# Kernel optimization log

Hardware: AMD Instinct MI355X
Metric: run time of the kernel (lower is better)

## Reference

```python
import jax, jax.numpy as jnp
import numpy as np

N_NODES = 50000
IN_DIM = 128
HID = 64
HEADS = 4
N_EDGES = 800000


def setup_inputs() -> dict:
    key = jax.random.key(0)
    ks = jax.random.split(key, 16)
    x = jax.random.normal(ks[0], (N_NODES, IN_DIM), dtype=jnp.float32)
    edge_index = jax.random.randint(ks[1], (2, N_EDGES), 0, N_NODES, dtype=jnp.int32)
    s = 0.1
    # layer 0: IN_DIM -> HEADS*HID (concat)
    W0 = jax.random.normal(ks[2], (IN_DIM, HEADS * HID), dtype=jnp.float32) * s
    a_src0 = jax.random.normal(ks[3], (HEADS, HID), dtype=jnp.float32) * s
    a_dst0 = jax.random.normal(ks[4], (HEADS, HID), dtype=jnp.float32) * s
    b0 = jnp.zeros((HEADS * HID,), dtype=jnp.float32)
    # layer 1: HEADS*HID -> HEADS*HID (concat)
    W1 = jax.random.normal(ks[5], (HEADS * HID, HEADS * HID), dtype=jnp.float32) * s
    a_src1 = jax.random.normal(ks[6], (HEADS, HID), dtype=jnp.float32) * s
    a_dst1 = jax.random.normal(ks[7], (HEADS, HID), dtype=jnp.float32) * s
    b1 = jnp.zeros((HEADS * HID,), dtype=jnp.float32)
    # layer 2: HEADS*HID -> HID (heads=1, concat=False)
    W2 = jax.random.normal(ks[8], (HEADS * HID, HID), dtype=jnp.float32) * s
    a_src2 = jax.random.normal(ks[9], (1, HID), dtype=jnp.float32) * s
    a_dst2 = jax.random.normal(ks[10], (1, HID), dtype=jnp.float32) * s
    b2 = jnp.zeros((HID,), dtype=jnp.float32)
    return {"x": x, "edge_index": edge_index,
            "W0": W0, "a_src0": a_src0, "a_dst0": a_dst0, "b0": b0,
            "W1": W1, "a_src1": a_src1, "a_dst1": a_dst1, "b1": b1,
            "W2": W2, "a_src2": a_src2, "a_dst2": a_dst2, "b2": b2}


def gat_conv(h_in, src, dst, W, a_src, a_dst, b, concat):
    """PyG-style GATConv (eval mode, self-loops already appended to src/dst)."""
    H, C = a_src.shape
    n = h_in.shape[0]
    h = (h_in @ W).reshape(n, H, C)                       # [N,H,C]
    alpha_s = jnp.sum(h * a_src[None], axis=-1)            # [N,H]
    alpha_d = jnp.sum(h * a_dst[None], axis=-1)            # [N,H]
    e = jax.nn.leaky_relu(alpha_s[src] + alpha_d[dst], 0.2)  # [E,H]
    # segment softmax over destination neighborhoods (numerically stable)
    m = jax.ops.segment_max(e, dst, num_segments=n)        # [N,H]
    m = jnp.where(jnp.isfinite(m), m, 0.0)
    ex = jnp.exp(e - m[dst])
    denom = jax.ops.segment_sum(ex, dst, num_segments=n)
    alpha = ex / (denom[dst] + 1e-16)                      # [E,H]
    msg = h[src] * alpha[:, :, None]                       # [E,H,C]
    out = jax.ops.segment_sum(msg, dst, num_segments=n)    # [N,H,C]
    out = out.reshape(n, H * C) if concat else out.mean(axis=1)
    return out + b


def reference(x, edge_index, W0, a_src0, a_dst0, b0, W1, a_src1, a_dst1, b1, W2, a_src2, a_dst2, b2):
    n = x.shape[0]
    loops = jnp.arange(n, dtype=edge_index.dtype)
    src = jnp.concatenate([edge_index[0], loops])  # add self-loops (PyG default)
    dst = jnp.concatenate([edge_index[1], loops])
    h = gat_conv(x, src, dst, W0, a_src0, a_dst0, b0, concat=True)
    h = jax.nn.elu(h)
    h = gat_conv(h, src, dst, W1, a_src1, a_dst1, b1, concat=True)
    h = jax.nn.elu(h)
    h = gat_conv(h, src, dst, W2, a_src2, a_dst2, b2, concat=False)
    return h  # [N, HID]
```

## Files before the change

### kernel.cpp

```cpp
#include <hip/hip_runtime.h>
#include <hip/hip_bf16.h>

typedef __hip_bfloat16 bf16;
typedef short s8v __attribute__((ext_vector_type(8)));
typedef float f32x4 __attribute__((ext_vector_type(4)));

__device__ __forceinline__ unsigned short f2bf_bits(float x) {
    union { bf16 h; unsigned short u; } v; v.h = __float2bfloat16(x); return v.u;
}
__device__ __forceinline__ float bfbits2f(unsigned short u) {
    union { unsigned u32; float f; } v; v.u32 = ((unsigned)u) << 16; return v.f;
}

template<typename T>
__device__ __forceinline__ void gload_lds16(const T* g, T* l) {
    __builtin_amdgcn_global_load_lds(
        (const __attribute__((address_space(1))) unsigned int*)g,
        (__attribute__((address_space(3))) unsigned int*)l, 16, 0, 0);
}

__device__ __forceinline__ uint4 load8(const bf16* p) { return *(const uint4*)p; }

__global__ void convert_kernel(const float* __restrict__ x, bf16* __restrict__ xb, int total4) {
    int i = blockIdx.x * blockDim.x + threadIdx.x;
    if (i >= total4) return;
    float4 f = *(const float4*)(x + (size_t)i * 4);
    union { uint2 u; unsigned short us[4]; } cv;
    cv.us[0] = f2bf_bits(f.x); cv.us[1] = f2bf_bits(f.y);
    cv.us[2] = f2bf_bits(f.z); cv.us[3] = f2bf_bits(f.w);
    *(uint2*)(xb + (size_t)i * 4) = cv.u;
}

__device__ __forceinline__ void tr1(const float* W, bf16* Wt, int idx, int K, int N) {
    int nn = idx / K, k = idx - nn * K;
    Wt[idx] = __float2bfloat16(W[(size_t)k * N + nn]);
}
__global__ void transpose_all_kernel(const float* __restrict__ W0, const float* __restrict__ W1,
                                     const float* __restrict__ W2, bf16* __restrict__ wt0,
                                     bf16* __restrict__ wt1, bf16* __restrict__ wt2) {
    int idx = blockIdx.x * blockDim.x + threadIdx.x;
    if (idx < 32768) tr1(W0, wt0, idx, 128, 256);
    else if (idx < 32768 + 65536) tr1(W1, wt1, idx - 32768, 256, 256);
    else if (idx < 32768 + 65536 + 16384) tr1(W2, wt2, idx - 98304, 256, 64);
}

__global__ void hist_kernel(const int* __restrict__ dst, int* counts, int E, int n) {
    int i = blockIdx.x * blockDim.x + threadIdx.x;
    if (i < E) {
        int d = dst[i];
        if ((unsigned)d < (unsigned)n) atomicAdd(&counts[d], 1);
    }
}

__global__ __launch_bounds__(1024) void scan_phase1(
        const int* __restrict__ counts, int* __restrict__ excl_out,
        int* __restrict__ blocksums, int n) {
    __shared__ int wsum[16];
    __shared__ int woff[16];
    int tid = threadIdx.x, lane = tid & 63, wid = tid >> 6;
    int i = blockIdx.x * 1024 + tid;
    int v = (i < n) ? counts[i] + 1 : 0;
    int incl = v;
    #pragma unroll
    for (int d = 1; d < 64; d <<= 1) {
        int t = __shfl_up(incl, d, 64);
        if (lane >= d) incl += t;
    }
    if (lane == 63) wsum[wid] = incl;
    __syncthreads();
    if (wid == 0) {
        int wv = (lane < 16) ? wsum[lane] : 0;
        int wincl = wv;
        #pragma unroll
        for (int d = 1; d < 16; d <<= 1) {
            int t = __shfl_up(wincl, d, 64);
            if (lane >= d) wincl += t;
        }
        if (lane < 16) woff[lane] = wincl - wv;
    }
    __syncthreads();
    if (i < n) excl_out[i] = woff[wid] + incl - v;
    if (tid == 1023) blocksums[blockIdx.x] = woff[15] + wsum[15];
}

__global__ __launch_bounds__(1024) void scan_phase2(
        const int* __restrict__ blocksums, int* __restrict__ row_ptr,
        int* __restrict__ cursor, int nb, int n) {
    int tid = threadIdx.x, lane = tid & 63;
    int i = blockIdx.x * 1024 + tid;
    int v = (lane < nb) ? blocksums[lane] : 0;
    int incl = v;
    #pragma unroll
    for (int d = 1; d < 64; d <<= 1) {
        int t = __shfl_up(incl, d, 64);
        if (lane >= d) incl += t;
    }
    int excl_lane = incl - v;
    int base = __shfl(excl_lane, blockIdx.x, 64);
    int total = __shfl(incl, nb - 1, 64);
    if (i < n) {
        int val = row_ptr[i] + base;
        row_ptr[i] = val;
        cursor[i] = val;
    }
    if (blockIdx.x == 0 && tid == 0) row_ptr[n] = total;
}

__global__ void scatter_kernel(const int* __restrict__ src, const int* __restrict__ dst,
                               int* cursor, int* col_src, int E, int n) {
    int i = blockIdx.x * blockDim.x + threadIdx.x;
    if (i < E) {
        int d = dst[i];
        if ((unsigned)d >= (unsigned)n) return;
        int s = src[i];
        if ((unsigned)s >= (unsigned)n) s = d;
        int pos = atomicAdd(&cursor[d], 1);
        col_src[pos] = s;
    } else if (i < E + n) {
        int v = i - E;
        int pos = atomicAdd(&cursor[v], 1);
        col_src[pos] = v;
    }
}

__global__ __launch_bounds__(256) void gemm128_kernel(
        const bf16* __restrict__ A, const bf16* __restrict__ Wt, bf16* __restrict__ C,
        const float* __restrict__ a_src, const float* __restrict__ a_dst,
        float* __restrict__ asb, float* __restrict__ adb,
        int M, int K, int N, int H) {
    __shared__ __align__(16) bf16 As[128 * 64];
    __shared__ __align__(16) bf16 Bs[128 * 64];
    int tid = threadIdx.x;
    int w = tid >> 6, l = tid & 63;
    int lm = l & 15, quad = l >> 4;
    int m0 = blockIdx.x * 128, n0 = blockIdx.y * 128;
    int wr = (w >> 1) * 64, wc = (w & 1) * 64;
    int srow = w * 32 + (l >> 3);
    int schunk = l & 7;
    f32x4 acc[4][4] = {};
    for (int kt = 0; kt < K; kt += 64) {
        #pragma unroll
        for (int j = 0; j < 4; ++j) {
            int row = srow + j * 8;
            int g = schunk ^ (row & 7);
            int m = m0 + row; if (m >= M) m = M - 1;
            gload_lds16(A + (size_t)m * K + kt + g * 8, As + row * 64 + schunk * 8);
            gload_lds16(Wt + (size_t)(n0 + row) * K + kt + g * 8, Bs + row * 64 + schunk * 8);
        }
        __syncthreads();
        #pragma unroll
        for (int ks = 0; ks < 2; ++ks) {
            s8v a[4], b[4];
            #pragma unroll
            for (int mi = 0; mi < 4; ++mi) {
                int row = wr + mi * 16 + lm;
                int c = (ks * 4 + quad) ^ (row & 7);
                a[mi] = *(const s8v*)(As + row * 64 + c * 8);
            }
            #pragma unroll
            for (int ni = 0; ni < 4; ++ni) {
                int row = wc + ni * 16 + lm;
                int c = (ks * 4 + quad) ^ (row & 7);
                b[ni] = *(const s8v*)(Bs + row * 64 + c * 8);
            }
            #pragma unroll
            for (int mi = 0; mi < 4; ++mi)
                #pragma unroll
                for (int ni = 0; ni < 4; ++ni)
                    acc[mi][ni] = __builtin_amdgcn_mfma_f32_16x16x32_bf16(
                        a[mi], b[ni], acc[mi][ni], 0, 0, 0);
        }
        __syncthreads();
    }
    int head = (n0 + wc) >> 6;
    float a_s[4], a_d[4];
    #pragma unroll
    for (int ni = 0; ni < 4; ++ni) {
        int col = n0 + wc + ni * 16 + lm;
        a_s[ni] = a_src[col];
        a_d[ni] = a_dst[col];
    }
    #pragma unroll
    for (int mi = 0; mi < 4; ++mi) {
        #pragma unroll
        for (int reg = 0; reg < 4; ++reg) {
            int m = m0 + wr + mi * 16 + quad * 4 + reg;
            float ps = 0.f, pd = 0.f;
            #pragma unroll
            for (int ni = 0; ni < 4; ++ni) {
                float v = acc[mi][ni][reg];
                ps += v * a_s[ni];
                pd += v * a_d[ni];
                if (m < M)
                    C[(size_t)m * N + n0 + wc + ni * 16 + lm] = __float2bfloat16(v);
            }
            #pragma unroll
            for (int d = 1; d < 16; d <<= 1) {
                ps += __shfl_xor(ps, d, 64);
                pd += __shfl_xor(pd, d, 64);
            }
            if (lm == 0 && m < M) {
                atomicAdd(&asb[(size_t)m * H + head], ps);
                atomicAdd(&adb[(size_t)m * H + head], pd);
            }
        }
    }
}

__global__ __launch_bounds__(256) void gemm64_kernel(
        const bf16* __restrict__ A, const bf16* __restrict__ Wt, bf16* __restrict__ C,
        const float* __restrict__ a_src, const float* __restrict__ a_dst,
        float* __restrict__ asb, float* __restrict__ adb,
        int M, int K, int N) {
    __shared__ __align__(16) bf16 As[64][72];
    __shared__ __align__(16) bf16 Bs[64][72];
    int tid = threadIdx.x;
    int m0 = blockIdx.x * 64;
    int w = tid >> 6;
    int l = tid & 63;
    int lm = l & 15;
    int quad = l >> 4;
    int r = tid >> 2;
    int kb = (tid & 3) * 8;
    f32x4 acc[4] = {};
    int mstage = m0 + r;
    for (int kt = 0; kt < K; kt += 64) {
        #pragma unroll
        for (int c = 0; c < 2; ++c) {
            int kk = kb + c * 32;
            uint4 av = (mstage < M) ? load8(&A[(size_t)mstage * K + kt + kk])
                                    : make_uint4(0, 0, 0, 0);
            *(uint4*)&As[r][kk] = av;
            *(uint4*)&Bs[r][kk] = load8(&Wt[(size_t)r * K + kt + kk]);
        }
        __syncthreads();
        #pragma unroll
        for (int ks = 0; ks < 2; ++ks) {
            s8v a = *(const s8v*)&As[w * 16 + lm][ks * 32 + quad * 8];
            #pragma unroll
            for (int nb = 0; nb < 4; ++nb) {
                s8v b = *(const s8v*)&Bs[nb * 16 + lm][ks * 32 + quad * 8];
                acc[nb] = __builtin_amdgcn_mfma_f32_16x16x32_bf16(a, b, acc[nb], 0, 0, 0);
            }
        }
        __syncthreads();
    }
    float a_s[4], a_d[4];
    #pragma unroll
    for (int nb = 0; nb < 4; ++nb) {
        a_s[nb] = a_src[nb * 16 + lm];
        a_d[nb] = a_dst[nb * 16 + lm];
    }
    #pragma unroll
    for (int reg = 0; reg < 4; ++reg) {
        int m = m0 + w * 16 + quad * 4 + reg;
        float ps = 0.f, pd = 0.f;
        #pragma unroll
        for (int nb = 0; nb < 4; ++nb) {
            float v = acc[nb][reg];
            ps += v * a_s[nb];
            pd += v * a_d[nb];
            if (m < M)
                C[(size_t)m * N + nb * 16 + lm] = __float2bfloat16(v);
        }
        #pragma unroll
        for (int d = 1; d < 16; d <<= 1) {
            ps += __shfl_xor(ps, d, 64);
            pd += __shfl_xor(pd, d, 64);
        }
        if (lm == 0 && m < M) {
            atomicAdd(&asb[m], ps);
            atomicAdd(&adb[m], pd);
        }
    }
}

template<int CTOT, int H, int VEC, typename TOUT>
__global__ __launch_bounds__(256) void agg_kernel(
        const bf16* __restrict__ hbuf,
        const float* __restrict__ as, const float* __restrict__ ad,
        const int* __restrict__ row_ptr, const int* __restrict__ col_src,
        const float* __restrict__ bias,
        TOUT* __restrict__ outp, int n, int apply_elu) {
    int lane = threadIdx.x & 63;
    int node = blockIdx.x * 4 + (threadIdx.x >> 6);
    if (node >= n) return;
    const int c0 = lane * VEC;
    const int head = c0 >> 6;
    int start = row_ptr[node], end = row_ptr[node + 1];
    float adn = ad[(size_t)node * H + head];
    float acc[VEC] = {};
    float denom = 0.f;

    auto edge_w = [&](int s) -> float {
        float x = as[(size_t)s * H + head] + adn;
        x = (x > 0.f) ? x : 0.2f * x;
        return __expf(fminf(x, 30.f));
    };
    auto loadH = [&](int s, float* o) {
        const bf16* p = hbuf + (size_t)s * CTOT + c0;
        if constexpr (VEC == 4) {
            union { uint2 u; unsigned short us[4]; } cv;
            cv.u = *(const uint2*)p;
            #pragma unroll
            for (int v = 0; v < 4; ++v) o[v] = bfbits2f(cv.us[v]);
        } else {
            o[0] = bfbits2f(*(const unsigned short*)p);
        }
    };

    int e = start;
    for (; e + 8 <= end; e += 8) {
        int s[8];
        float w[8], hv[8][VEC];
        #pragma unroll
        for (int j = 0; j < 8; ++j) {
            s[j] = col_src[e + j];
            if ((unsigned)s[j] >= (unsigned)n) s[j] = node;
        }
        #pragma unroll
        for (int j = 0; j < 8; ++j) loadH(s[j], hv[j]);
        #pragma unroll
        for (int j = 0; j < 8; ++j) w[j] = edge_w(s[j]);
        #pragma unroll
        for (int j = 0; j < 8; ++j) {
            denom += w[j];
            #pragma unroll
            for (int v = 0; v < VEC; ++v) acc[v] += w[j] * hv[j][v];
        }
    }
    for (; e < end; ++e) {
        int s = col_src[e];
        if ((unsigned)s >= (unsigned)n) s = node;
        float hv[VEC];
        loadH(s, hv);
        float w = edge_w(s);
        denom += w;
        #pragma unroll
        for (int v = 0; v < VEC; ++v) acc[v] += w * hv[v];
    }
    float inv = 1.f / (denom + 1e-16f);
    float o[VEC];
    #pragma unroll
    for (int v = 0; v < VEC; ++v) {
        o[v] = acc[v] * inv + bias[c0 + v];
        if (apply_elu) o[v] = (o[v] > 0.f) ? o[v] : (__expf(o[v]) - 1.f);
    }
    if constexpr (VEC == 4) {
        union { uint2 u; unsigned short us[4]; } cv;
        #pragma unroll
        for (int v = 0; v < 4; ++v) cv.us[v] = f2bf_bits(o[v]);
        *(uint2*)((bf16*)outp + (size_t)node * CTOT + c0) = cv.u;
    } else {
        outp[(size_t)node * CTOT + c0] = (TOUT)o[0];
    }
}

extern "C" void kernel_launch(void* const* d_in, const int* in_sizes, int n_in,
                              void* d_out, int out_size, void* d_ws, size_t ws_size,
                              hipStream_t stream) {
    const float* x   = (const float*)d_in[0];
    const int*   ei  = (const int*)d_in[1];
    const float* W0  = (const float*)d_in[2];
    const float* as0 = (const float*)d_in[3];
    const float* ad0 = (const float*)d_in[4];
    const float* b0  = (const float*)d_in[5];
    const float* W1  = (const float*)d_in[6];
    const float* as1 = (const float*)d_in[7];
    const float* ad1 = (const float*)d_in[8];
    const float* b1  = (const float*)d_in[9];
    const float* W2  = (const float*)d_in[10];
    const float* as2 = (const float*)d_in[11];
    const float* ad2 = (const float*)d_in[12];
    const float* b2  = (const float*)d_in[13];
    float* out = (float*)d_out;

    const int n = in_sizes[0] / 128;
    const int E = in_sizes[1] / 2;
    const int* esrc = ei;
    const int* edst = ei + E;

    char* ws = (char*)d_ws;
    bf16* hb0 = (bf16*)ws;
    bf16* hb1 = hb0 + (size_t)n * 256;
    bf16* xb  = hb1 + (size_t)n * 256;
    bf16* wt0 = xb + (size_t)n * 128;
    bf16* wt1 = wt0 + 128 * 256;
    bf16* wt2 = wt1 + 256 * 256;
    float* asb = (float*)(wt2 + 256 * 64);
    float* adb = asb + (size_t)n * 4;
    int* row_ptr = (int*)(adb + (size_t)n * 4);
    int* cursor  = row_ptr + (n + 64);
    int* col_src = cursor + n;
    int* blocksums = col_src + (E + n + 64);

    const int nb = (n + 1023) / 1024;

    convert_kernel<<<(n * 128 / 4 + 255) / 256, 256, 0, stream>>>(x, xb, n * 128 / 4);
    transpose_all_kernel<<<(114688 + 255) / 256, 256, 0, stream>>>(W0, W1, W2, wt0, wt1, wt2);
    hipMemsetAsync(cursor, 0, (size_t)n * sizeof(int), stream);
    hist_kernel<<<(E + 255) / 256, 256, 0, stream>>>(edst, cursor, E, n);
    scan_phase1<<<nb, 1024, 0, stream>>>(cursor, row_ptr, blocksums, n);
    scan_phase2<<<nb, 1024, 0, stream>>>(blocksums, row_ptr, cursor, nb, n);
    scatter_kernel<<<(E + n + 255) / 256, 256, 0, stream>>>(esrc, edst, cursor, col_src, E, n);

    dim3 blk(256);
    int mg128 = (n + 127) / 128;
    int mg64  = (n + 63) / 64;
    int ag = (n + 3) / 4;
    size_t alpha_bytes = (size_t)n * 8 * sizeof(float);

    hipMemsetAsync(asb, 0, alpha_bytes, stream);
    gemm128_kernel<<<dim3(mg128, 2), blk, 0, stream>>>(xb, wt0, hb0, as0, ad0,
                                                       asb, adb, n, 128, 256, 4);
    agg_kernel<256, 4, 4, bf16><<<ag, blk, 0, stream>>>(hb0, asb, adb, row_ptr, col_src,
                                                        b0, hb1, n, 1);
    hipMemsetAsync(asb, 0, alpha_bytes, stream);
    gemm128_kernel<<<dim3(mg128, 2), blk, 0, stream>>>(hb1, wt1, hb0, as1, ad1,
                                                       asb, adb, n, 256, 256, 4);
    agg_kernel<256, 4, 4, bf16><<<ag, blk, 0, stream>>>(hb0, asb, adb, row_ptr, col_src,
                                                        b1, hb1, n, 1);
    hipMemsetAsync(asb, 0, alpha_bytes, stream);
    gemm64_kernel<<<dim3(mg64, 1), blk, 0, stream>>>(hb1, wt2, hb0, as2, ad2,
                                                     asb, adb, n, 256, 64);
    agg_kernel<64, 1, 1, float><<<ag, blk, 0, stream>>>(hb0, asb, adb, row_ptr, col_src,
                                                        b2, out, n, 0);
}
```

Before: 476.9 us.

## Precompute per-edge attention weights in a separate pass before aggregation

Adds a wprep kernel that computes the leaky-ReLU/exp edge weight once per edge and head and stores it in a buffer aliased over the bf16 input copy. Previously every lane of the aggregation kernel gathered the source alpha and recomputed the exponential itself. The aggregation now reads these precomputed weights, and its unroll factor drops from 8 to 4 when each lane holds 4 channels. The cost is an extra launch per layer plus writing and re-reading about (E+N)*H floats, while the source-alpha gathers it replaces were small and likely cache-resident.

```diff
diff --git a/kernel.cpp b/kernel.cpp
--- a/kernel.cpp
+++ b/kernel.cpp
@@ -275,10 +275,33 @@
     }
 }
 
+template<int H>
+__global__ __launch_bounds__(256) void wprep_kernel(
+        const float* __restrict__ asb, const float* __restrict__ adb,
+        const int* __restrict__ row_ptr, const int* __restrict__ col_src,
+        float* __restrict__ wge, int n) {
+    int lane = threadIdx.x & 63;
+    int node = blockIdx.x * 4 + (threadIdx.x >> 6);
+    if (node >= n) return;
+    int start = row_ptr[node], end = row_ptr[node + 1];
+    float adn[H];
+    #pragma unroll
+    for (int h = 0; h < H; ++h) adn[h] = adb[(size_t)node * H + h];
+    for (int e = start + lane; e < end; e += 64) {
+        int s = col_src[e];
+        if ((unsigned)s >= (unsigned)n) s = node;
+        #pragma unroll
+        for (int h = 0; h < H; ++h) {
+            float x = asb[(size_t)s * H + h] + adn[h];
+            x = (x > 0.f) ? x : 0.2f * x;
+            wge[(size_t)e * H + h] = __expf(fminf(x, 30.f));
+        }
+    }
+}
+
 template<int CTOT, int H, int VEC, typename TOUT>
 __global__ __launch_bounds__(256) void agg_kernel(
-        const bf16* __restrict__ hbuf,
-        const float* __restrict__ as, const float* __restrict__ ad,
+        const bf16* __restrict__ hbuf, const float* __restrict__ wge,
         const int* __restrict__ row_ptr, const int* __restrict__ col_src,
         const float* __restrict__ bias,
         TOUT* __restrict__ outp, int n, int apply_elu) {
@@ -288,15 +311,9 @@
     const int c0 = lane * VEC;
     const int head = c0 >> 6;
     int start = row_ptr[node], end = row_ptr[node + 1];
-    float adn = ad[(size_t)node * H + head];
     float acc[VEC] = {};
     float denom = 0.f;
 
-    auto edge_w = [&](int s) -> float {
-        float x = as[(size_t)s * H + head] + adn;
-        x = (x > 0.f) ? x : 0.2f * x;
-        return __expf(fminf(x, 30.f));
-    };
     auto loadH = [&](int s, float* o) {
         const bf16* p = hbuf + (size_t)s * CTOT + c0;
         if constexpr (VEC == 4) {
@@ -309,21 +326,22 @@
         }
     };
 
+    constexpr int U = (VEC == 1) ? 8 : 4;
     int e = start;
-    for (; e + 8 <= end; e += 8) {
-        int s[8];
-        float w[8], hv[8][VEC];
-        #pragma unroll
-        for (int j = 0; j < 8; ++j) {
+    for (; e + U <= end; e += U) {
+        int s[U];
+        float w[U], hv[U][VEC];
+        #pragma unroll
+        for (int j = 0; j < U; ++j) {
             s[j] = col_src[e + j];
             if ((unsigned)s[j] >= (unsigned)n) s[j] = node;
         }
         #pragma unroll
-        for (int j = 0; j < 8; ++j) loadH(s[j], hv[j]);
-        #pragma unroll
-        for (int j = 0; j < 8; ++j) w[j] = edge_w(s[j]);
-        #pragma unroll
-        for (int j = 0; j < 8; ++j) {
+        for (int j = 0; j < U; ++j) w[j] = wge[(size_t)(e + j) * H + head];
+        #pragma unroll
+        for (int j = 0; j < U; ++j) loadH(s[j], hv[j]);
+        #pragma unroll
+        for (int j = 0; j < U; ++j) {
             denom += w[j];
             #pragma unroll
             for (int v = 0; v < VEC; ++v) acc[v] += w[j] * hv[j][v];
@@ -334,7 +352,7 @@
         if ((unsigned)s >= (unsigned)n) s = node;
         float hv[VEC];
         loadH(s, hv);
-        float w = edge_w(s);
+        float w = wge[(size_t)e * H + head];
         denom += w;
         #pragma unroll
         for (int v = 0; v < VEC; ++v) acc[v] += w * hv[v];
@@ -384,7 +402,9 @@
     bf16* hb0 = (bf16*)ws;
     bf16* hb1 = hb0 + (size_t)n * 256;
     bf16* xb  = hb1 + (size_t)n * 256;
-    bf16* wt0 = xb + (size_t)n * 128;
+    float* wge = (float*)xb;
+    char* after_xw = (char*)xb + ((size_t)(E + n + 64) * 4 * sizeof(float));
+    bf16* wt0 = (bf16*)after_xw;
     bf16* wt1 = wt0 + 128 * 256;
     bf16* wt2 = wt1 + 256 * 256;
     float* asb = (float*)(wt2 + 256 * 64);
@@ -413,16 +433,19 @@
     hipMemsetAsync(asb, 0, alpha_bytes, stream);
     gemm128_kernel<<<dim3(mg128, 2), blk, 0, stream>>>(xb, wt0, hb0, as0, ad0,
                                                        asb, adb, n, 128, 256, 4);
-    agg_kernel<256, 4, 4, bf16><<<ag, blk, 0, stream>>>(hb0, asb, adb, row_ptr, col_src,
+    wprep_kernel<4><<<ag, blk, 0, stream>>>(asb, adb, row_ptr, col_src, wge, n);
+    agg_kernel<256, 4, 4, bf16><<<ag, blk, 0, stream>>>(hb0, wge, row_ptr, col_src,
                                                         b0, hb1, n, 1);
     hipMemsetAsync(asb, 0, alpha_bytes, stream);
     gemm128_kernel<<<dim3(mg128, 2), blk, 0, stream>>>(hb1, wt1, hb0, as1, ad1,
                                                        asb, adb, n, 256, 256, 4);
-    agg_kernel<256, 4, 4, bf16><<<ag, blk, 0, stream>>>(hb0, asb, adb, row_ptr, col_src,
+    wprep_kernel<4><<<ag, blk, 0, stream>>>(asb, adb, row_ptr, col_src, wge, n);
+    agg_kernel<256, 4, 4, bf16><<<ag, blk, 0, stream>>>(hb0, wge, row_ptr, col_src,
                                                         b1, hb1, n, 1);
     hipMemsetAsync(asb, 0, alpha_bytes, stream);
     gemm64_kernel<<<dim3(mg64, 1), blk, 0, stream>>>(hb1, wt2, hb0, as2, ad2,
                                                      asb, adb, n, 256, 64);
-    agg_kernel<64, 1, 1, float><<<ag, blk, 0, stream>>>(hb0, asb, adb, row_ptr, col_src,
+    wprep_kernel<1><<<ag, blk, 0, stream>>>(asb, adb, row_ptr, col_src, wge, n);
+    agg_kernel<64, 1, 1, float><<<ag, blk, 0, stream>>>(hb0, wge, row_ptr, col_src,
                                                         b2, out, n, 0);
 }
```

New measurement: 476.8 us. About the same (-0.0%).

## Share edge weights across lanes in aggregation, drop alpha atomics and memsets

Applied to the files above, without the earlier changes.

The aggregation kernel now has each lane compute the attention weight for one edge of a batch and broadcasts it with shuffles, instead of every lane recomputing exp for every edge. GEMM epilogues write attention logits with plain stores rather than atomics, removing the zeroing memsets. Input conversion, weight transposes and cursor zeroing are merged into one prep kernel. The gather loop no longer clamps out-of-range source indices, and correctness relies on each logit being written by exactly one wave.

```diff
diff --git a/kernel.cpp b/kernel.cpp
--- a/kernel.cpp
+++ b/kernel.cpp
@@ -21,27 +21,32 @@
 
 __device__ __forceinline__ uint4 load8(const bf16* p) { return *(const uint4*)p; }
 
-__global__ void convert_kernel(const float* __restrict__ x, bf16* __restrict__ xb, int total4) {
-    int i = blockIdx.x * blockDim.x + threadIdx.x;
-    if (i >= total4) return;
-    float4 f = *(const float4*)(x + (size_t)i * 4);
-    union { uint2 u; unsigned short us[4]; } cv;
-    cv.us[0] = f2bf_bits(f.x); cv.us[1] = f2bf_bits(f.y);
-    cv.us[2] = f2bf_bits(f.z); cv.us[3] = f2bf_bits(f.w);
-    *(uint2*)(xb + (size_t)i * 4) = cv.u;
-}
-
 __device__ __forceinline__ void tr1(const float* W, bf16* Wt, int idx, int K, int N) {
     int nn = idx / K, k = idx - nn * K;
     Wt[idx] = __float2bfloat16(W[(size_t)k * N + nn]);
 }
-__global__ void transpose_all_kernel(const float* __restrict__ W0, const float* __restrict__ W1,
-                                     const float* __restrict__ W2, bf16* __restrict__ wt0,
-                                     bf16* __restrict__ wt1, bf16* __restrict__ wt2) {
+__global__ void prep_kernel(const float* __restrict__ x, bf16* __restrict__ xb, int nc4,
+                            const float* __restrict__ W0, const float* __restrict__ W1,
+                            const float* __restrict__ W2, bf16* __restrict__ wt0,
+                            bf16* __restrict__ wt1, bf16* __restrict__ wt2,
+                            int* __restrict__ cursor, int n) {
     int idx = blockIdx.x * blockDim.x + threadIdx.x;
-    if (idx < 32768) tr1(W0, wt0, idx, 128, 256);
-    else if (idx < 32768 + 65536) tr1(W1, wt1, idx - 32768, 256, 256);
-    else if (idx < 32768 + 65536 + 16384) tr1(W2, wt2, idx - 98304, 256, 64);
+    if (idx < nc4) {
+        float4 f = *(const float4*)(x + (size_t)idx * 4);
+        union { uint2 u; unsigned short us[4]; } cv;
+        cv.us[0] = f2bf_bits(f.x); cv.us[1] = f2bf_bits(f.y);
+        cv.us[2] = f2bf_bits(f.z); cv.us[3] = f2bf_bits(f.w);
+        *(uint2*)(xb + (size_t)idx * 4) = cv.u;
+        return;
+    }
+    int i2 = idx - nc4;
+    if (i2 < 32768) { tr1(W0, wt0, i2, 128, 256); return; }
+    i2 -= 32768;
+    if (i2 < 65536) { tr1(W1, wt1, i2, 256, 256); return; }
+    i2 -= 65536;
+    if (i2 < 16384) { tr1(W2, wt2, i2, 256, 64); return; }
+    i2 -= 16384;
+    if (i2 < n) cursor[i2] = 0;
 }
 
 __global__ void hist_kernel(const int* __restrict__ dst, int* counts, int E, int n) {
@@ -200,8 +205,8 @@
                 pd += __shfl_xor(pd, d, 64);
             }
             if (lm == 0 && m < M) {
-                atomicAdd(&asb[(size_t)m * H + head], ps);
-                atomicAdd(&adb[(size_t)m * H + head], pd);
+                asb[(size_t)m * H + head] = ps;
+                adb[(size_t)m * H + head] = pd;
             }
         }
     }
@@ -269,8 +274,8 @@
             pd += __shfl_xor(pd, d, 64);
         }
         if (lm == 0 && m < M) {
-            atomicAdd(&asb[m], ps);
-            atomicAdd(&adb[m], pd);
+            asb[m] = ps;
+            adb[m] = pd;
         }
     }
 }
@@ -278,25 +283,22 @@
 template<int CTOT, int H, int VEC, typename TOUT>
 __global__ __launch_bounds__(256) void agg_kernel(
         const bf16* __restrict__ hbuf,
-        const float* __restrict__ as, const float* __restrict__ ad,
+        const float* __restrict__ asb, const float* __restrict__ adb,
         const int* __restrict__ row_ptr, const int* __restrict__ col_src,
         const float* __restrict__ bias,
         TOUT* __restrict__ outp, int n, int apply_elu) {
+    constexpr int BATCH = 64 / H;
     int lane = threadIdx.x & 63;
     int node = blockIdx.x * 4 + (threadIdx.x >> 6);
     if (node >= n) return;
     const int c0 = lane * VEC;
-    const int head = c0 >> 6;
+    const int head = lane / BATCH;
+    const int sub = lane % BATCH;
     int start = row_ptr[node], end = row_ptr[node + 1];
-    float adn = ad[(size_t)node * H + head];
+    float adn = adb[(size_t)node * H + head];
     float acc[VEC] = {};
     float denom = 0.f;
 
-    auto edge_w = [&](int s) -> float {
-        float x = as[(size_t)s * H + head] + adn;
-        x = (x > 0.f) ? x : 0.2f * x;
-        return __expf(fminf(x, 30.f));
-    };
     auto loadH = [&](int s, float* o) {
         const bf16* p = hbuf + (size_t)s * CTOT + c0;
         if constexpr (VEC == 4) {
@@ -309,35 +311,40 @@
         }
     };
 
-    int e = start;
-    for (; e + 8 <= end; e += 8) {
-        int s[8];
-        float w[8], hv[8][VEC];
-        #pragma unroll
-        for (int j = 0; j < 8; ++j) {
-            s[j] = col_src[e + j];
-            if ((unsigned)s[j] >= (unsigned)n) s[j] = node;
-        }
-        #pragma unroll
-        for (int j = 0; j < 8; ++j) loadH(s[j], hv[j]);
-        #pragma unroll
-        for (int j = 0; j < 8; ++j) w[j] = edge_w(s[j]);
-        #pragma unroll
-        for (int j = 0; j < 8; ++j) {
-            denom += w[j];
-            #pragma unroll
-            for (int v = 0; v < VEC; ++v) acc[v] += w[j] * hv[j][v];
-        }
-    }
-    for (; e < end; ++e) {
-        int s = col_src[e];
-        if ((unsigned)s >= (unsigned)n) s = node;
-        float hv[VEC];
-        loadH(s, hv);
-        float w = edge_w(s);
-        denom += w;
-        #pragma unroll
-        for (int v = 0; v < VEC; ++v) acc[v] += w * hv[v];
+    for (int base = start; base < end; base += BATCH) {
+        int nbatch = end - base;
+        if (nbatch > BATCH) nbatch = BATCH;
+        float wv = 0.f;
+        if (sub < nbatch) {
+            int s = col_src[base + sub];
+            float xv = asb[(size_t)s * H + head] + adn;
+            xv = (xv > 0.f) ? xv : 0.2f * xv;
+            wv = __expf(fminf(xv, 30.f));
+        }
+        int j = 0;
+        for (; j + 4 <= nbatch; j += 4) {
+            int s0 = col_src[base + j], s1 = col_src[base + j + 1];
+            int s2 = col_src[base + j + 2], s3 = col_src[base + j + 3];
+            float hv0[VEC], hv1[VEC], hv2[VEC], hv3[VEC];
+            loadH(s0, hv0); loadH(s1, hv1); loadH(s2, hv2); loadH(s3, hv3);
+            float w0 = __shfl(wv, head * BATCH + j, 64);
+            float w1 = __shfl(wv, head * BATCH + j + 1, 64);
+            float w2 = __shfl(wv, head * BATCH + j + 2, 64);
+            float w3 = __shfl(wv, head * BATCH + j + 3, 64);
+            denom += (w0 + w1) + (w2 + w3);
+            #pragma unroll
+            for (int v = 0; v < VEC; ++v)
+                acc[v] += w0 * hv0[v] + w1 * hv1[v] + w2 * hv2[v] + w3 * hv3[v];
+        }
+        for (; j < nbatch; ++j) {
+            int s = col_src[base + j];
+            float hv[VEC];
+            loadH(s, hv);
+            float wj = __shfl(wv, head * BATCH + j, 64);
+            denom += wj;
+            #pragma unroll
+            for (int v = 0; v < VEC; ++v) acc[v] += wj * hv[v];
+        }
     }
     float inv = 1.f / (denom + 1e-16f);
     float o[VEC];
@@ -395,10 +402,11 @@
     int* blocksums = col_src + (E + n + 64);
 
     const int nb = (n + 1023) / 1024;
-
-    convert_kernel<<<(n * 128 / 4 + 255) / 256, 256, 0, stream>>>(x, xb, n * 128 / 4);
-    transpose_all_kernel<<<(114688 + 255) / 256, 256, 0, stream>>>(W0, W1, W2, wt0, wt1, wt2);
-    hipMemsetAsync(cursor, 0, (size_t)n * sizeof(int), stream);
+    const int nc4 = n * 128 / 4;
+
+    int prep_threads = nc4 + 114688 + n;
+    prep_kernel<<<(prep_threads + 255) / 256, 256, 0, stream>>>(
+        x, xb, nc4, W0, W1, W2, wt0, wt1, wt2, cursor, n);
     hist_kernel<<<(E + 255) / 256, 256, 0, stream>>>(edst, cursor, E, n);
     scan_phase1<<<nb, 1024, 0, stream>>>(cursor, row_ptr, blocksums, n);
     scan_phase2<<<nb, 1024, 0, stream>>>(blocksums, row_ptr, cursor, nb, n);
@@ -408,19 +416,15 @@
     int mg128 = (n + 127) / 128;
     int mg64  = (n + 63) / 64;
     int ag = (n + 3) / 4;
-    size_t alpha_bytes = (size_t)n * 8 * sizeof(float);
-
-    hipMemsetAsync(asb, 0, alpha_bytes, stream);
+
     gemm128_kernel<<<dim3(mg128, 2), blk, 0, stream>>>(xb, wt0, hb0, as0, ad0,
                                                        asb, adb, n, 128, 256, 4);
     agg_kernel<256, 4, 4, bf16><<<ag, blk, 0, stream>>>(hb0, asb, adb, row_ptr, col_src,
                                                         b0, hb1, n, 1);
-    hipMemsetAsync(asb, 0, alpha_bytes, stream);
     gemm128_kernel<<<dim3(mg128, 2), blk, 0, stream>>>(hb1, wt1, hb0, as1, ad1,
                                                        asb, adb, n, 256, 256, 4);
     agg_kernel<256, 4, 4, bf16><<<ag, blk, 0, stream>>>(hb0, asb, adb, row_ptr, col_src,
                                                         b1, hb1, n, 1);
-    hipMemsetAsync(asb, 0, alpha_bytes, stream);
     gemm64_kernel<<<dim3(mg64, 1), blk, 0, stream>>>(hb1, wt2, hb0, as2, ad2,
                                                      asb, adb, n, 256, 64);
     agg_kernel<64, 1, 1, float><<<ag, blk, 0, stream>>>(hb0, asb, adb, row_ptr, col_src,
```

Result: faster. 429.0 us (-10.0%).
